# Performance work log

Measured on AMD Instinct MI355X. Metric: run time of the kernel, lower is better.

Reference implementation:

```python
import jax, jax.numpy as jnp
import numpy as np

DIM = 4096
N_HEADS = 32
N_KV_HEADS = 8
HEAD_DIM = DIM // N_HEADS  # 128
B, S = 1, 2048
ROPE_THETA = 10000.0


def setup_inputs() -> dict:
    key = jax.random.key(0)
    kx, kq, kk, kv, ko = jax.random.split(key, 5)
    x = jax.random.normal(kx, (B, S, DIM), dtype=jnp.float32)
    # torch Linear weights are [out_features, in_features]
    wq = jax.random.normal(kq, (N_HEADS * HEAD_DIM, DIM), dtype=jnp.float32) * 0.02
    wk = jax.random.normal(kk, (N_KV_HEADS * HEAD_DIM, DIM), dtype=jnp.float32) * 0.02
    wv = jax.random.normal(kv, (N_KV_HEADS * HEAD_DIM, DIM), dtype=jnp.float32) * 0.02
    wo = jax.random.normal(ko, (DIM, N_HEADS * HEAD_DIM), dtype=jnp.float32) * 0.02
    # RoPE table [S, HEAD_DIM, 2]; frequencies repeated twice to match the
    # even/odd interleaved rotate_half convention of apply_rope.
    pos = jnp.arange(S, dtype=jnp.float32)
    inv_freq = 1.0 / (ROPE_THETA ** (jnp.arange(0, HEAD_DIM, 2, dtype=jnp.float32) / HEAD_DIM))
    ang = pos[:, None] * inv_freq[None, :]          # [S, HEAD_DIM/2]
    ang = jnp.repeat(ang, 2, axis=-1)               # [S, HEAD_DIM]
    rope_freqs = jnp.stack([jnp.cos(ang), jnp.sin(ang)], axis=-1)  # [S, HEAD_DIM, 2]
    return {"x": x, "wq": wq, "wk": wk, "wv": wv, "wo": wo,
            "rope_freqs": rope_freqs, "start_pos": 0}


def _rotate_half(t):
    # interleaved: (x0,x1,x2,x3,...) -> (-x1,x0,-x3,x2,...)
    t1 = t[..., ::2]
    t2 = t[..., 1::2]
    return jnp.stack((-t2, t1), axis=-1).reshape(t.shape)


def reference(x, wq, wk, wv, wo, rope_freqs, start_pos):
    b, s, _ = x.shape
    rep = N_HEADS // N_KV_HEADS
    scale = 1.0 / np.sqrt(HEAD_DIM)

    q = (x @ wq.T).reshape(b, s, N_HEADS, HEAD_DIM)
    k = (x @ wk.T).reshape(b, s, N_KV_HEADS, HEAD_DIM)
    v = (x @ wv.T).reshape(b, s, N_KV_HEADS, HEAD_DIM)

    cos = rope_freqs[..., 0][None, :, None, :]  # [1,S,1,HEAD_DIM]
    sin = rope_freqs[..., 1][None, :, None, :]
    q = q * cos + _rotate_half(q) * sin
    k = k * cos + _rotate_half(k) * sin

    # GQA without materializing repeated K/V: group query heads by kv head.
    qg = q.reshape(b, s, N_KV_HEADS, rep, HEAD_DIM)
    scores = jnp.einsum("bsgrd,btgd->bgrst", qg, k) * scale  # [B,KV,rep,S,S]
    causal = jnp.tril(jnp.ones((s, s), dtype=bool))
    scores = jnp.where(causal, scores, jnp.finfo(scores.dtype).min)
    attn = jax.nn.softmax(scores, axis=-1)
    out = jnp.einsum("bgrst,btgd->bsgrd", attn, v)           # [B,S,KV,rep,HEAD_DIM]
    out = out.reshape(b, s, N_HEADS * HEAD_DIM)
    return out @ wo.T
```

## Files before the change

kernel.cpp:

```cpp
#include <hip/hip_runtime.h>
#include <stdint.h>

#define DIM 4096
#define NH 32
#define NKV 8
#define HD 128
#define SEQ 2048
#define KVD 1024

typedef unsigned short u16;
typedef __attribute__((ext_vector_type(8))) short bf16x8;
typedef __attribute__((ext_vector_type(4))) float f32x4;

__device__ __forceinline__ float bf2f(u16 v){
  union { unsigned u; float f; } c; c.u = ((unsigned)v) << 16; return c.f;
}
__device__ __forceinline__ u16 f2bf(float f){
  union { float f; unsigned u; } c; c.f = f;
  unsigned u = c.u;
  u += 0x7FFF + ((u >> 16) & 1);
  return (u16)(u >> 16);
}
__device__ __forceinline__ unsigned pack2bf(float a, float b){
  return (unsigned)f2bf(a) | ((unsigned)f2bf(b) << 16);
}

__device__ __forceinline__ void gl_lds16(const void* g, void* l){
  __builtin_amdgcn_global_load_lds((const __attribute__((address_space(1))) void*)g,
                                   (__attribute__((address_space(3))) void*)l, 16, 0, 0);
}

#define VM4 asm volatile("s_waitcnt vmcnt(4)" ::: "memory")
#define VM0 asm volatile("s_waitcnt vmcnt(0)" ::: "memory")
#define BAR __builtin_amdgcn_s_barrier()

__global__ void cvt_all(const float* __restrict__ x,  const float* __restrict__ wq,
                        const float* __restrict__ wk, const float* __restrict__ wv,
                        const float* __restrict__ wo,
                        u16* __restrict__ xb,  u16* __restrict__ wqb,
                        u16* __restrict__ wkb, u16* __restrict__ wvb,
                        u16* __restrict__ wob){
  const int b = blockIdx.x;
  const float* in; u16* out; int base;
  if      (b <  8192){ in = x;  out = xb;  base = b; }
  else if (b < 24576){ in = wq; out = wqb; base = b - 8192; }
  else if (b < 28672){ in = wk; out = wkb; base = b - 24576; }
  else if (b < 32768){ in = wv; out = wvb; base = b - 28672; }
  else               { in = wo; out = wob; base = b - 32768; }
  const int i = (base*256 + threadIdx.x)*4;
  float4 v = *(const float4*)(in + i);
  ushort4 o;
  o.x = f2bf(v.x); o.y = f2bf(v.y); o.z = f2bf(v.z); o.w = f2bf(v.w);
  *(ushort4*)(out + i) = o;
}

__global__ void add_f32(float* __restrict__ out, const float* __restrict__ p){
  const int i = blockIdx.x*256 + threadIdx.x;
  float4 a = ((const float4*)out)[i];
  const float4 b = ((const float4*)p)[i];
  a.x += b.x; a.y += b.y; a.z += b.z; a.w += b.w;
  ((float4*)out)[i] = a;
}

template<int EPI>
__global__ __launch_bounds__(512, 2) void gemm256(const u16* __restrict__ A,
    const u16* __restrict__ B0, const u16* __restrict__ B1, const u16* __restrict__ B2,
    void* __restrict__ C0, void* __restrict__ C1, void* __restrict__ C2,
    const float* __restrict__ rf){
  __shared__ __align__(16) char lds[131072];
  const int t = threadIdx.x, w = t >> 6, l = t & 63;
  const int lg = l >> 4, li = l & 15;
  const int wr = w >> 2, wc = w & 3;
  const int nwg = gridDim.x;
  const int idx = ((int)blockIdx.x & 7)*(nwg >> 3) + ((int)blockIdx.x >> 3);

  int bm, bn, kbase, nt, ks = 0;
  const u16 *Ab, *Bb;
  if (EPI == 0){
    bm = idx & 7; bn = idx >> 3;
    kbase = 0; nt = 64;
    Ab = A + (size_t)bm*256*DIM;
    Bb = (bn < 16) ? B0 + (size_t)bn*256*DIM
       : (bn < 20) ? B1 + (size_t)(bn-16)*256*DIM
                   : B2 + (size_t)(bn-20)*256*DIM;
  } else {
    bm = idx & 7; ks = (idx >> 3) & 1; bn = idx >> 4;
    kbase = ks*2048; nt = 32;
    Ab = A + (size_t)bm*256*DIM;
    Bb = B0 + (size_t)bn*256*DIM;
  }

  auto stHalf = [&](const u16* P, int rowbase, int kabs, int ldsoff){
    #pragma unroll
    for (int jj = 0; jj < 2; ++jj){
      const int rloc = jj*64 + (t >> 3);
      const int row  = rowbase + rloc;
      gl_lds16(P + (size_t)row*DIM + kabs + (((t & 7) ^ (row & 7)) << 3),
               lds + ldsoff + rloc*128 + (t & 7)*16);
    }
  };

  f32x4 acc[8][4] = {};

#define PHASE(H, G) { \
    bf16x8 a_[4][2], b_[2][2]; \
    _Pragma("unroll") \
    for (int i2 = 0; i2 < 4; ++i2){ \
      const int R = (H)*128 + wr*64 + i2*16 + li; \
      a_[i2][0] = *(const bf16x8*)(ldsA + R*128 + (( lg    ^ (R & 7)) << 4)); \
      a_[i2][1] = *(const bf16x8*)(ldsA + R*128 + (((lg+4) ^ (R & 7)) << 4)); \
    } \
    _Pragma("unroll") \
    for (int j2 = 0; j2 < 2; ++j2){ \
      const int R = (G)*128 + wc*32 + j2*16 + li; \
      b_[j2][0] = *(const bf16x8*)(ldsB + R*128 + (( lg    ^ (R & 7)) << 4)); \
      b_[j2][1] = *(const bf16x8*)(ldsB + R*128 + (((lg+4) ^ (R & 7)) << 4)); \
    } \
    __builtin_amdgcn_s_setprio(1); \
    _Pragma("unroll") \
    for (int i2 = 0; i2 < 4; ++i2) \
      _Pragma("unroll") \
      for (int j2 = 0; j2 < 2; ++j2){ \
        acc[(H)*4+i2][(G)*2+j2] = __builtin_amdgcn_mfma_f32_16x16x32_bf16(a_[i2][0], b_[j2][0], acc[(H)*4+i2][(G)*2+j2], 0, 0, 0); \
        acc[(H)*4+i2][(G)*2+j2] = __builtin_amdgcn_mfma_f32_16x16x32_bf16(a_[i2][1], b_[j2][1], acc[(H)*4+i2][(G)*2+j2], 0, 0, 0); \
      } \
    __builtin_amdgcn_s_setprio(0); \
  }

  stHalf(Ab,   0, kbase,         0);
  stHalf(Bb,   0, kbase, 65536    );
  stHalf(Ab, 128, kbase,     16384);
  stHalf(Bb, 128, kbase, 65536+16384);

  for (int tt = 0; tt < nt; ++tt){
    const int buf = tt & 1, b2 = buf ^ 1;
    const int k1 = kbase + (tt+1)*64;
    const bool pf = (tt + 1 < nt);
    const char* ldsA = lds + buf*32768;
    const char* ldsB = lds + 65536 + buf*32768;
    const int a2 = b2*32768, bo2 = 65536 + b2*32768;

    if (pf) VM4; else VM0;
    BAR;
    if (pf) stHalf(Ab, 0, k1, a2);
    PHASE(0, 0)
    if (pf) VM4;
    BAR;
    if (pf) stHalf(Bb, 0, k1, bo2);
    PHASE(1, 0)
    if (pf) VM4;
    BAR;
    if (pf) stHalf(Ab, 128, k1, a2 + 16384);
    PHASE(0, 1)
    if (pf) stHalf(Bb, 128, k1, bo2 + 16384);
    PHASE(1, 1)
  }
#undef PHASE

  if (EPI == 1){
    float* C = (float*)(ks ? C1 : C0);
    #pragma unroll
    for (int i = 0; i < 8; ++i){
      const int srow = bm*256 + ((i < 4) ? wr*64 + i*16 : 128 + wr*64 + (i-4)*16) + lg*4;
      #pragma unroll
      for (int j = 0; j < 4; ++j){
        const int col = bn*256 + ((j < 2) ? wc*32 + j*16 : 128 + wc*32 + (j-2)*16) + li;
        #pragma unroll
        for (int r = 0; r < 4; ++r)
          C[(size_t)(srow + r)*DIM + col] = acc[i][j][r];
      }
    }
  } else {
    if (bn < 20){
      u16* C = (bn < 16) ? (u16*)C0 : (u16*)C1;
      const int ldc = (bn < 16) ? DIM : KVD;
      const int cb  = (bn < 16) ? bn*256 : (bn-16)*256;
      #pragma unroll
      for (int i = 0; i < 8; ++i){
        const int srow0 = bm*256 + ((i < 4) ? wr*64 + i*16 : 128 + wr*64 + (i-4)*16) + lg*4;
        #pragma unroll
        for (int j = 0; j < 4; ++j){
          const int col = cb + ((j < 2) ? wc*32 + j*16 : 128 + wc*32 + (j-2)*16) + li;
          const int i4 = ((col & 127) >> 1) << 2;
          #pragma unroll
          for (int r = 0; r < 4; ++r){
            const float v = acc[i][j][r];
            const float p = __shfl_xor(v, 1);
            const int srow = srow0 + r;
            const float cs = rf[(size_t)srow*256 + i4];
            const float sn = rf[(size_t)srow*256 + i4 + 1];
            const float o = (col & 1) ? (v*cs + p*sn) : (v*cs - p*sn);
            C[(size_t)srow*ldc + col] = f2bf(o);
          }
        }
      }
    } else {
      u16* C = (u16*)C2;
      const int cb = (bn - 20)*256;
      #pragma unroll
      for (int i = 0; i < 8; ++i){
        const int srow0 = bm*256 + ((i < 4) ? wr*64 + i*16 : 128 + wr*64 + (i-4)*16) + lg*4;
        #pragma unroll
        for (int j = 0; j < 4; ++j){
          const int col = cb + ((j < 2) ? wc*32 + j*16 : 128 + wc*32 + (j-2)*16) + li;
          ushort4 o;
          o.x = f2bf(acc[i][j][0]); o.y = f2bf(acc[i][j][1]);
          o.z = f2bf(acc[i][j][2]); o.w = f2bf(acc[i][j][3]);
          *(ushort4*)&C[(size_t)col*SEQ + srow0] = o;
        }
      }
    }
  }
}

__global__ __launch_bounds__(256) void flash_attn(const u16* __restrict__ Q,
                                                  const u16* __restrict__ Kg,
                                                  const u16* __restrict__ Vt,
                                                  u16* __restrict__ O){
  __shared__ bf16x8 smK[2][64*16];
  __shared__ bf16x8 smV[2][128*8];
  __shared__ __align__(16) u16 smP[4][16*64];
  const int bid = blockIdx.x;
  const int h  = bid & 31;
  const int qt = 31 - (bid >> 5);
  const int g  = h >> 2;
  const int t = threadIdx.x, w = t >> 6, l = t & 63;
  const int lg = l >> 4, li = l & 15;

  bf16x8 qf[4];
  {
    const u16* qrow = Q + (size_t)(qt*64 + w*16 + li)*DIM + h*HD;
    #pragma unroll
    for (int kc = 0; kc < 4; ++kc)
      qf[kc] = *(const bf16x8*)(qrow + kc*32 + lg*8);
  }
  f32x4 accO[8] = {};
  float mrun = -1e30f, lsum = 0.f;
  const float SC = 0.08838834764831845f * 1.4426950408889634f;

  const int ksrow = t >> 4, ksslot = t & 15;
  const int vsrow = t >> 3, vsslot = t & 7;

  auto stage = [&](int kt, int b){
    #pragma unroll
    for (int j = 0; j < 4; ++j){
      const int krow = j*16 + ksrow;
      const int ksl = (ksslot & 8) | ((ksslot ^ (krow & 7)) & 7);
      gl_lds16(Kg + (size_t)(kt*64 + krow)*KVD + g*HD + ksl*8, (char*)&smK[b][0] + j*4096 + w*1024);
      const int vrow = j*32 + vsrow;
      const int vsl = (vsslot ^ (vrow & 7)) & 7;
      gl_lds16(Vt + (size_t)(g*HD + vrow)*SEQ + kt*64 + vsl*8, (char*)&smV[b][0] + j*4096 + w*1024);
    }
  };

  stage(0, 0);
  int buf = 0;
  u16* pw = &smP[w][0];

  for (int kt = 0; kt <= qt; ++kt){
    __syncthreads();
    if (kt < qt) stage(kt + 1, buf ^ 1);

    f32x4 sacc[4] = {};
    #pragma unroll
    for (int kc = 0; kc < 4; ++kc){
      #pragma unroll
      for (int nj = 0; nj < 4; ++nj){
        const int R = nj*16 + li;
        int sl = lg + 4*kc;
        sl = (sl & 8) | ((sl ^ (R & 7)) & 7);
        sacc[nj] = __builtin_amdgcn_mfma_f32_16x16x32_bf16(smK[buf][R*16 + sl], qf[kc], sacc[nj], 0, 0, 0);
      }
    }
    float p[4][4];
    #pragma unroll
    for (int nj = 0; nj < 4; ++nj)
      #pragma unroll
      for (int r = 0; r < 4; ++r)
        p[nj][r] = sacc[nj][r] * SC;
    if (kt == qt){
      const int qloc = w*16 + li;
      #pragma unroll
      for (int nj = 0; nj < 4; ++nj)
        #pragma unroll
        for (int r = 0; r < 4; ++r)
          if (nj*16 + lg*4 + r > qloc) p[nj][r] = -1e30f;
    }
    float mx = p[0][0];
    #pragma unroll
    for (int nj = 0; nj < 4; ++nj)
      #pragma unroll
      for (int r = 0; r < 4; ++r) mx = fmaxf(mx, p[nj][r]);
    mx = fmaxf(mx, __shfl_xor(mx, 16));
    mx = fmaxf(mx, __shfl_xor(mx, 32));
    const float mnew = fmaxf(mrun, mx);
    const float alpha = exp2f(mrun - mnew);
    float s = 0.f;
    #pragma unroll
    for (int nj = 0; nj < 4; ++nj)
      #pragma unroll
      for (int r = 0; r < 4; ++r){ p[nj][r] = exp2f(p[nj][r] - mnew); s += p[nj][r]; }
    s += __shfl_xor(s, 16);
    s += __shfl_xor(s, 32);
    lsum = lsum * alpha + s;
    mrun = mnew;
    float al[4];
    #pragma unroll
    for (int r = 0; r < 4; ++r) al[r] = __shfl(alpha, (l & 48) | (lg*4 + r));
    #pragma unroll
    for (int dj = 0; dj < 8; ++dj)
      #pragma unroll
      for (int r = 0; r < 4; ++r) accO[dj][r] *= al[r];
    #pragma unroll
    for (int nj = 0; nj < 4; ++nj){
      const int c = nj*2 + (lg >> 1);
      uint2 v; v.x = pack2bf(p[nj][0], p[nj][1]); v.y = pack2bf(p[nj][2], p[nj][3]);
      *(uint2*)((char*)pw + li*128 + ((c ^ (li & 7)) << 4) + ((lg & 1) << 3)) = v;
    }
    #pragma unroll
    for (int kc2 = 0; kc2 < 2; ++kc2){
      const bf16x8 pf = *(const bf16x8*)((char*)pw + li*128 + (((kc2*4 + lg) ^ (li & 7)) << 4));
      #pragma unroll
      for (int dj = 0; dj < 8; ++dj){
        const int R = dj*16 + li;
        const bf16x8 vf = smV[buf][R*8 + ((lg + 4*kc2) ^ (R & 7))];
        accO[dj] = __builtin_amdgcn_mfma_f32_16x16x32_bf16(pf, vf, accO[dj], 0, 0, 0);
      }
    }
    buf ^= 1;
  }
  float linv[4];
  #pragma unroll
  for (int r = 0; r < 4; ++r) linv[r] = 1.f / __shfl(lsum, (l & 48) | (lg*4 + r));
  #pragma unroll
  for (int dj = 0; dj < 8; ++dj)
    #pragma unroll
    for (int r = 0; r < 4; ++r)
      O[(size_t)(qt*64 + w*16 + lg*4 + r)*DIM + h*HD + dj*16 + li] = f2bf(accO[dj][r] * linv[r]);
}

extern "C" void kernel_launch(void* const* d_in, const int* in_sizes, int n_in,
                              void* d_out, int out_size, void* d_ws, size_t ws_size,
                              hipStream_t stream){
  const float* x  = (const float*)d_in[0];
  const float* wq = (const float*)d_in[1];
  const float* wk = (const float*)d_in[2];
  const float* wv = (const float*)d_in[3];
  const float* wo = (const float*)d_in[4];
  const float* rf = (const float*)d_in[5];
  float* out = (float*)d_out;

  char* ws = (char*)d_ws;
  size_t off = 0;
  auto alloc = [&](size_t nbytes){ void* p = ws + off; off += (nbytes + 255) & ~(size_t)255; return p; };
  u16* xb  = (u16*)alloc((size_t)SEQ*DIM*2);
  u16* wqb = (u16*)alloc((size_t)DIM*DIM*2);
  u16* wkb = (u16*)alloc((size_t)KVD*DIM*2);
  u16* wvb = (u16*)alloc((size_t)KVD*DIM*2);
  u16* wob = (u16*)alloc((size_t)DIM*DIM*2);
  u16* Qb  = (u16*)alloc((size_t)SEQ*DIM*2);
  u16* K8  = (u16*)alloc((size_t)SEQ*KVD*2);
  u16* Vtr = (u16*)alloc((size_t)KVD*SEQ*2);
  u16* AO  = (u16*)alloc((size_t)SEQ*DIM*2);
  float* P1 = (float*)wqb;

  cvt_all<<<49152, 256, 0, stream>>>(x, wq, wk, wv, wo, xb, wqb, wkb, wvb, wob);

  gemm256<0><<<192, 512, 0, stream>>>(xb, wqb, wkb, wvb, Qb, K8, Vtr, rf);

  flash_attn<<<SEQ/64 * NH, 256, 0, stream>>>(Qb, K8, Vtr, AO);

  gemm256<1><<<256, 512, 0, stream>>>(AO, wob, nullptr, nullptr, out, P1, nullptr, nullptr);
  add_f32<<<8192, 256, 0, stream>>>(out, P1);
}
```

Measured before the change: 334.4 us.

## Retile QKV GEMM to 256x192 blocks and restructure the K-loop pipeline

Replaces the 256x256 GEMM with a templated kernel whose N-tile width is set by BUNITS. The fused QKV projection uses 256x192 tiles, which gives 256 workgroups instead of 192, so the grid fills all CUs. It treats wq/wk/wv as one contiguous 6144-row B matrix, relying on the workspace allocations sitting back to back. The K-loop is reorganised into four phases. Each phase issues its prefetch, waits at a barrier and on LDS counters, then runs the MFMAs, and B fragments are held in registers across phases. This adds more barriers per iteration and a layout dependency between the weight buffers.

```diff
diff --git a/kernel.cpp b/kernel.cpp
--- a/kernel.cpp
+++ b/kernel.cpp
@@ -31,7 +31,10 @@
 }
 
 #define VM4 asm volatile("s_waitcnt vmcnt(4)" ::: "memory")
+#define VM2 asm volatile("s_waitcnt vmcnt(2)" ::: "memory")
 #define VM0 asm volatile("s_waitcnt vmcnt(0)" ::: "memory")
+#define LGKM0 asm volatile("s_waitcnt lgkmcnt(0)" ::: "memory")
+#define SB0 __builtin_amdgcn_sched_barrier(0)
 #define BAR __builtin_amdgcn_s_barrier()
 
 __global__ void cvt_all(const float* __restrict__ x,  const float* __restrict__ wq,
@@ -62,125 +65,115 @@
   ((float4*)out)[i] = a;
 }
 
-template<int EPI>
-__global__ __launch_bounds__(512, 2) void gemm256(const u16* __restrict__ A,
-    const u16* __restrict__ B0, const u16* __restrict__ B1, const u16* __restrict__ B2,
-    void* __restrict__ C0, void* __restrict__ C1, void* __restrict__ C2,
-    const float* __restrict__ rf){
-  __shared__ __align__(16) char lds[131072];
+template<int BUNITS, int EPI>
+__global__ __launch_bounds__(512, 2) void gemmP(const u16* __restrict__ A,
+    const u16* __restrict__ B, void* __restrict__ C0, void* __restrict__ C1,
+    void* __restrict__ C2, const float* __restrict__ rf, float* __restrict__ Cp){
+  constexpr int BN = BUNITS*64;
+  __shared__ __align__(16) char lds[65536 + BUNITS*16384];
   const int t = threadIdx.x, w = t >> 6, l = t & 63;
   const int lg = l >> 4, li = l & 15;
   const int wr = w >> 2, wc = w & 3;
-  const int nwg = gridDim.x;
-  const int idx = ((int)blockIdx.x & 7)*(nwg >> 3) + ((int)blockIdx.x >> 3);
+  const int idx = ((int)blockIdx.x & 7)*32 + ((int)blockIdx.x >> 3);
 
   int bm, bn, kbase, nt, ks = 0;
-  const u16 *Ab, *Bb;
-  if (EPI == 0){
-    bm = idx & 7; bn = idx >> 3;
-    kbase = 0; nt = 64;
-    Ab = A + (size_t)bm*256*DIM;
-    Bb = (bn < 16) ? B0 + (size_t)bn*256*DIM
-       : (bn < 20) ? B1 + (size_t)(bn-16)*256*DIM
-                   : B2 + (size_t)(bn-20)*256*DIM;
-  } else {
-    bm = idx & 7; ks = (idx >> 3) & 1; bn = idx >> 4;
-    kbase = ks*2048; nt = 32;
-    Ab = A + (size_t)bm*256*DIM;
-    Bb = B0 + (size_t)bn*256*DIM;
-  }
-
-  auto stHalf = [&](const u16* P, int rowbase, int kabs, int ldsoff){
-    #pragma unroll
-    for (int jj = 0; jj < 2; ++jj){
-      const int rloc = jj*64 + (t >> 3);
-      const int row  = rowbase + rloc;
-      gl_lds16(P + (size_t)row*DIM + kabs + (((t & 7) ^ (row & 7)) << 3),
-               lds + ldsoff + rloc*128 + (t & 7)*16);
-    }
+  if (EPI == 0){ bm = idx & 7; bn = idx >> 3; kbase = 0; nt = 64; }
+  else         { bm = idx & 7; ks = (idx >> 3) & 1; bn = idx >> 4; kbase = ks*2048; nt = 32; }
+  const u16* Ab = A + (size_t)bm*256*DIM;
+  const u16* Bb = B + (size_t)bn*BN*DIM;
+
+  auto stA = [&](int k0, int abase, int u){
+    const int r = u*64 + (t >> 3);
+    gl_lds16(Ab + (size_t)r*DIM + k0 + (((t & 7) ^ (r & 7)) << 3),
+             lds + abase + u*8192 + (t >> 3)*128 + (t & 7)*16);
   };
-
-  f32x4 acc[8][4] = {};
-
-#define PHASE(H, G) { \
-    bf16x8 a_[4][2], b_[2][2]; \
+  auto stB = [&](int k0, int bbase, int u){
+    const int r = u*64 + (t >> 3);
+    gl_lds16(Bb + (size_t)r*DIM + k0 + (((t & 7) ^ (r & 7)) << 3),
+             lds + bbase + u*8192 + (t >> 3)*128 + (t & 7)*16);
+  };
+
+  f32x4 acc[8][BUNITS] = {};
+  bf16x8 bfr[BUNITS][2];
+
+#define PH(p, ...) { \
+    bf16x8 af[2][2]; \
     _Pragma("unroll") \
-    for (int i2 = 0; i2 < 4; ++i2){ \
-      const int R = (H)*128 + wr*64 + i2*16 + li; \
-      a_[i2][0] = *(const bf16x8*)(ldsA + R*128 + (( lg    ^ (R & 7)) << 4)); \
-      a_[i2][1] = *(const bf16x8*)(ldsA + R*128 + (((lg+4) ^ (R & 7)) << 4)); \
+    for (int q = 0; q < 2; ++q){ \
+      const int R = wr*128 + (2*(p)+q)*16 + li; \
+      af[q][0] = *(const bf16x8*)(ldsA + R*128 + (( lg    ^ (R & 7)) << 4)); \
+      af[q][1] = *(const bf16x8*)(ldsA + R*128 + (((lg+4) ^ (R & 7)) << 4)); \
     } \
-    _Pragma("unroll") \
-    for (int j2 = 0; j2 < 2; ++j2){ \
-      const int R = (G)*128 + wc*32 + j2*16 + li; \
-      b_[j2][0] = *(const bf16x8*)(ldsB + R*128 + (( lg    ^ (R & 7)) << 4)); \
-      b_[j2][1] = *(const bf16x8*)(ldsB + R*128 + (((lg+4) ^ (R & 7)) << 4)); \
+    if ((p) == 0){ \
+      _Pragma("unroll") \
+      for (int j = 0; j < BUNITS; ++j){ \
+        const int R = wc*(BUNITS*16) + j*16 + li; \
+        bfr[j][0] = *(const bf16x8*)(ldsB + R*128 + (( lg    ^ (R & 7)) << 4)); \
+        bfr[j][1] = *(const bf16x8*)(ldsB + R*128 + (((lg+4) ^ (R & 7)) << 4)); \
+      } \
     } \
+    __VA_ARGS__; \
+    BAR; LGKM0; SB0; \
     __builtin_amdgcn_s_setprio(1); \
     _Pragma("unroll") \
-    for (int i2 = 0; i2 < 4; ++i2) \
+    for (int q = 0; q < 2; ++q) \
       _Pragma("unroll") \
-      for (int j2 = 0; j2 < 2; ++j2){ \
-        acc[(H)*4+i2][(G)*2+j2] = __builtin_amdgcn_mfma_f32_16x16x32_bf16(a_[i2][0], b_[j2][0], acc[(H)*4+i2][(G)*2+j2], 0, 0, 0); \
-        acc[(H)*4+i2][(G)*2+j2] = __builtin_amdgcn_mfma_f32_16x16x32_bf16(a_[i2][1], b_[j2][1], acc[(H)*4+i2][(G)*2+j2], 0, 0, 0); \
+      for (int j = 0; j < BUNITS; ++j){ \
+        acc[2*(p)+q][j] = __builtin_amdgcn_mfma_f32_16x16x32_bf16(af[q][0], bfr[j][0], acc[2*(p)+q][j], 0, 0, 0); \
+        acc[2*(p)+q][j] = __builtin_amdgcn_mfma_f32_16x16x32_bf16(af[q][1], bfr[j][1], acc[2*(p)+q][j], 0, 0, 0); \
       } \
     __builtin_amdgcn_s_setprio(0); \
-  }
-
-  stHalf(Ab,   0, kbase,         0);
-  stHalf(Bb,   0, kbase, 65536    );
-  stHalf(Ab, 128, kbase,     16384);
-  stHalf(Bb, 128, kbase, 65536+16384);
+    BAR; }
+
+  stA(kbase, 0, 0); stA(kbase, 0, 2);
+  #pragma unroll
+  for (int u = 0; u < BUNITS; ++u) stB(kbase, 65536, u);
+  stA(kbase, 0, 1); stA(kbase, 0, 3);
+  VM2; BAR;
 
   for (int tt = 0; tt < nt; ++tt){
     const int buf = tt & 1, b2 = buf ^ 1;
     const int k1 = kbase + (tt+1)*64;
     const bool pf = (tt + 1 < nt);
     const char* ldsA = lds + buf*32768;
-    const char* ldsB = lds + 65536 + buf*32768;
-    const int a2 = b2*32768, bo2 = 65536 + b2*32768;
-
-    if (pf) VM4; else VM0;
-    BAR;
-    if (pf) stHalf(Ab, 0, k1, a2);
-    PHASE(0, 0)
-    if (pf) VM4;
-    BAR;
-    if (pf) stHalf(Bb, 0, k1, bo2);
-    PHASE(1, 0)
-    if (pf) VM4;
-    BAR;
-    if (pf) stHalf(Ab, 128, k1, a2 + 16384);
-    PHASE(0, 1)
-    if (pf) stHalf(Bb, 128, k1, bo2 + 16384);
-    PHASE(1, 1)
+    const char* ldsB = lds + 65536 + buf*BUNITS*8192;
+    const int a2 = b2*32768, b2o = 65536 + b2*BUNITS*8192;
+
+    PH(0, if (pf){ stA(k1, a2, 0); stA(k1, a2, 2); })
+    PH(1, if (pf){ stB(k1, b2o, 0); stB(k1, b2o, 1); VM4; } else { VM0; })
+    PH(2, if (pf){ if constexpr (BUNITS == 4){ stB(k1, b2o, 2); stB(k1, b2o, 3); }
+                   else                      { stB(k1, b2o, 2); stA(k1, a2, 1); } })
+    PH(3, if (pf){ if constexpr (BUNITS == 4){ stA(k1, a2, 1); stA(k1, a2, 3); }
+                   else                      { stA(k1, a2, 3); }
+                   VM2; })
   }
-#undef PHASE
+#undef PH
 
   if (EPI == 1){
-    float* C = (float*)(ks ? C1 : C0);
+    float* C = (float*)(ks ? Cp : C0);
     #pragma unroll
     for (int i = 0; i < 8; ++i){
-      const int srow = bm*256 + ((i < 4) ? wr*64 + i*16 : 128 + wr*64 + (i-4)*16) + lg*4;
-      #pragma unroll
-      for (int j = 0; j < 4; ++j){
-        const int col = bn*256 + ((j < 2) ? wc*32 + j*16 : 128 + wc*32 + (j-2)*16) + li;
+      const int srow = bm*256 + wr*128 + i*16 + lg*4;
+      #pragma unroll
+      for (int j = 0; j < BUNITS; ++j){
+        const int col = bn*BN + wc*(BUNITS*16) + j*16 + li;
         #pragma unroll
         for (int r = 0; r < 4; ++r)
           C[(size_t)(srow + r)*DIM + col] = acc[i][j][r];
       }
     }
   } else {
-    if (bn < 20){
-      u16* C = (bn < 16) ? (u16*)C0 : (u16*)C1;
-      const int ldc = (bn < 16) ? DIM : KVD;
-      const int cb  = (bn < 16) ? bn*256 : (bn-16)*256;
-      #pragma unroll
-      for (int i = 0; i < 8; ++i){
-        const int srow0 = bm*256 + ((i < 4) ? wr*64 + i*16 : 128 + wr*64 + (i-4)*16) + lg*4;
-        #pragma unroll
-        for (int j = 0; j < 4; ++j){
-          const int col = cb + ((j < 2) ? wc*32 + j*16 : 128 + wc*32 + (j-2)*16) + li;
+    #pragma unroll
+    for (int i = 0; i < 8; ++i){
+      const int srow0 = bm*256 + wr*128 + i*16 + lg*4;
+      #pragma unroll
+      for (int j = 0; j < BUNITS; ++j){
+        const int fc0 = bn*BN + wc*(BUNITS*16) + j*16;
+        const int col = fc0 + li;
+        if (fc0 < 5120){
+          u16* C  = (fc0 < 4096) ? (u16*)C0 : (u16*)C1;
+          const int ldc  = (fc0 < 4096) ? DIM : KVD;
+          const int ccol = (fc0 < 4096) ? col : col - 4096;
           const int i4 = ((col & 127) >> 1) << 2;
           #pragma unroll
           for (int r = 0; r < 4; ++r){
@@ -190,23 +183,14 @@
             const float cs = rf[(size_t)srow*256 + i4];
             const float sn = rf[(size_t)srow*256 + i4 + 1];
             const float o = (col & 1) ? (v*cs + p*sn) : (v*cs - p*sn);
-            C[(size_t)srow*ldc + col] = f2bf(o);
+            C[(size_t)srow*ldc + ccol] = f2bf(o);
           }
-        }
-      }
-    } else {
-      u16* C = (u16*)C2;
-      const int cb = (bn - 20)*256;
-      #pragma unroll
-      for (int i = 0; i < 8; ++i){
-        const int srow0 = bm*256 + ((i < 4) ? wr*64 + i*16 : 128 + wr*64 + (i-4)*16) + lg*4;
-        #pragma unroll
-        for (int j = 0; j < 4; ++j){
-          const int col = cb + ((j < 2) ? wc*32 + j*16 : 128 + wc*32 + (j-2)*16) + li;
+        } else {
+          u16* C = (u16*)C2;
           ushort4 o;
           o.x = f2bf(acc[i][j][0]); o.y = f2bf(acc[i][j][1]);
           o.z = f2bf(acc[i][j][2]); o.w = f2bf(acc[i][j][3]);
-          *(ushort4*)&C[(size_t)col*SEQ + srow0] = o;
+          *(ushort4*)&C[(size_t)(col - 5120)*SEQ + srow0] = o;
         }
       }
     }
@@ -366,10 +350,10 @@
 
   cvt_all<<<49152, 256, 0, stream>>>(x, wq, wk, wv, wo, xb, wqb, wkb, wvb, wob);
 
-  gemm256<0><<<192, 512, 0, stream>>>(xb, wqb, wkb, wvb, Qb, K8, Vtr, rf);
+  gemmP<3, 0><<<256, 512, 0, stream>>>(xb, wqb, Qb, K8, Vtr, rf, nullptr);
 
   flash_attn<<<SEQ/64 * NH, 256, 0, stream>>>(Qb, K8, Vtr, AO);
 
-  gemm256<1><<<256, 512, 0, stream>>>(AO, wob, nullptr, nullptr, out, P1, nullptr, nullptr);
+  gemmP<4, 1><<<256, 512, 0, stream>>>(AO, wob, out, nullptr, nullptr, nullptr, P1);
   add_f32<<<8192, 256, 0, stream>>>(out, P1);
 }
```

Measured after the change: 314.5 us. 1.06x faster.
